# Performance work log

Measured on AMD Instinct MI355X. Metric: run time of the kernel, lower is better.

## Reference

```python
import jax, jax.numpy as jnp
import numpy as np
from jax.scipy.special import logsumexp

D = 256; H = 8; A = D // H
B_CONST = 0.9; P_MAX = 50000.0; P_MIN = 1e-4; TANH_RATE = 0.005; EPS = 1e-10
SCALE = 1.0 / np.sqrt(D)


def setup_inputs() -> dict:
    key = jax.random.key(0)
    ks = jax.random.split(key, 5)
    B, S = 2, 512
    context = jax.random.normal(ks[0], (B, S, D), dtype=jnp.float32)
    W_Q = jax.random.normal(ks[1], (D, D), dtype=jnp.float32) * (1.0 / np.sqrt(D))
    W_KV = jax.random.normal(ks[2], (2 * D, D), dtype=jnp.float32) * (1.0 / np.sqrt(D))
    W_out = jax.random.normal(ks[3], (D, D), dtype=jnp.float32) * (1.0 / np.sqrt(D))
    p_param = jax.random.normal(ks[4], (D,), dtype=jnp.float32) * 0.02
    return {"context": context, "W_Q": W_Q, "W_KV": W_KV, "W_out": W_out, "p_param": p_param}


def reference(context, W_Q, W_KV, W_out, p_param):
    B, S, _ = context.shape
    # projections (nn.Linear: x @ W.T)
    q = context @ W_Q.T                          # [B,S,D]
    kv = context @ W_KV.T                        # [B,S,2D]
    k, v = kv[..., :D], kv[..., D:]
    # scaled p: p_max*tanh(tanh_rate*p)+1, then replace exact zeros with p_min
    p = P_MAX * jnp.tanh(TANH_RATE * p_param) + 1.0
    p = p + (p == 0).astype(p.dtype) * P_MIN
    # minmax-normalize v over the key/sequence axis into [b, 1]
    v_max = jnp.max(v, axis=-2, keepdims=True)   # [B,1,D]
    v_min = jnp.min(v, axis=-2, keepdims=True)
    v = (1.0 - B_CONST) * (v - v_min) / (v_max - v_min + EPS) + B_CONST
    z = p * jnp.log(v)                           # [B,S,D]
    # split heads
    qh = q.reshape(B, S, H, A).transpose(0, 2, 1, 3)          # [B,H,S,A]
    kh = k.reshape(B, S, H, A).transpose(0, 2, 1, 3)          # [B,H,S,A]
    zh = z.reshape(B, S, H, A).transpose(0, 2, 1, 3)[:, :, None]  # [B,H,1,K,A]
    dot = jnp.einsum('bhqa,bhka->bhqk', qh, kh)
    w = jax.nn.log_softmax(dot * SCALE, axis=-1)              # [B,H,Q,K]
    # log-domain power mean: logsumexp over keys of log-weights + p*log(v)
    mean = logsumexp(w[..., None] + zh, axis=-2)              # [B,H,Q,A]
    mean = mean.transpose(0, 2, 1, 3).reshape(B, S, D)
    e = jnp.exp(mean / p)
    # invert v minmax normalization
    e = (e - B_CONST) * (v_max - v_min + EPS) / (1.0 - B_CONST) + v_min
    return e @ W_out.T
```

## Files before the change

kernel.cpp:

```cpp
#include <hip/hip_runtime.h>
#include <math.h>

#define DD 256
#define HH 8
#define AA 32
#define SS 512
#define BB 2
constexpr float BCONST      = 0.9f;
constexpr float ONE_MINUS_B = 0.1f;
constexpr float EPSF        = 1e-10f;
constexpr float SCALEF      = 0.0625f;
constexpr float FLTMAX      = 3.402823466e38f;

#define OFF_QKV    0
#define OFF_VP     786432
#define OFF_EW     1048576
#define OFF_PMIN   1310720
#define OFF_PMAX   1318912
#define OFF_VMIN   1327104
#define OFF_VRANGE 1327616
#define OFF_P      1328128

#define KB4(buf, row, col4) \
  (&(buf)[((row) << 5) | ((((col4) >> 2) ^ (((row) >> 2) & 7)) << 2)])

template<int TM, int TN, int RM, int RN, bool MM>
__global__ __launch_bounds__(256) void gemm_t(
    const float* __restrict__ A, const float* __restrict__ B0,
    const float* __restrict__ B1, int nsplit,
    float* __restrict__ C, int ldc, int K, int lda,
    float* __restrict__ pminP, float* __restrict__ pmaxP) {
  constexpr int LDT = 36;
  constexpr int CG  = TN / RN;
  constexpr int NA  = TM * 32 / 1024;
  constexpr int NB  = TN * 32 / 1024;
  __shared__ float As[TM][LDT];
  __shared__ float Bs[TN][LDT];
  const int i0 = blockIdx.x * TM;
  const int j0 = blockIdx.y * TN;
  const float* Bsrc = (j0 < nsplit) ? (B0 + (size_t)j0 * K)
                                    : (B1 + (size_t)(j0 - nsplit) * K);
  const int t  = threadIdx.x;
  const int lr = t >> 3;
  const int lc = (t & 7) << 2;
  const int tx = t % CG, ty = t / CG;

  float4 pa[NA], pb[NB];
#pragma unroll
  for (int u = 0; u < NA; ++u)
    pa[u] = *(const float4*)(A + (size_t)(i0 + lr + 32 * u) * lda + lc);
#pragma unroll
  for (int u = 0; u < NB; ++u)
    pb[u] = *(const float4*)(Bsrc + (size_t)(lr + 32 * u) * K + lc);

  float acc[RM][RN] = {};
  for (int k0 = 0; k0 < K; k0 += 32) {
    __syncthreads();
#pragma unroll
    for (int u = 0; u < NA; ++u) *(float4*)&As[lr + 32 * u][lc] = pa[u];
#pragma unroll
    for (int u = 0; u < NB; ++u) *(float4*)&Bs[lr + 32 * u][lc] = pb[u];
    __syncthreads();
    if (k0 + 32 < K) {
#pragma unroll
      for (int u = 0; u < NA; ++u)
        pa[u] = *(const float4*)(A + (size_t)(i0 + lr + 32 * u) * lda + k0 + 32 + lc);
#pragma unroll
      for (int u = 0; u < NB; ++u)
        pb[u] = *(const float4*)(Bsrc + (size_t)(lr + 32 * u) * K + k0 + 32 + lc);
    }
#pragma unroll
    for (int kk = 0; kk < 32; kk += 4) {
      float4 af[RM], bf[RN];
#pragma unroll
      for (int r = 0; r < RM; ++r) af[r] = *(const float4*)&As[ty * RM + r][kk];
#pragma unroll
      for (int c = 0; c < RN; ++c) bf[c] = *(const float4*)&Bs[tx + CG * c][kk];
#pragma unroll
      for (int r = 0; r < RM; ++r)
#pragma unroll
        for (int c = 0; c < RN; ++c)
          acc[r][c] += af[r].x * bf[c].x + af[r].y * bf[c].y +
                       af[r].z * bf[c].z + af[r].w * bf[c].w;
    }
  }
#pragma unroll
  for (int r = 0; r < RM; ++r)
#pragma unroll
    for (int c = 0; c < RN; ++c)
      C[(size_t)(i0 + ty * RM + r) * ldc + j0 + tx + CG * c] = acc[r][c];

  if (MM && j0 >= 512) {
    __syncthreads();
    float* mnb = &As[0][0];
    float* mxb = &Bs[0][0];
#pragma unroll
    for (int c = 0; c < RN; ++c) {
      float mn = acc[0][c], mx = acc[0][c];
#pragma unroll
      for (int r = 1; r < RM; ++r) {
        mn = fminf(mn, acc[r][c]);
        mx = fmaxf(mx, acc[r][c]);
      }
      mnb[(tx + CG * c) * 17 + ty] = mn;
      mxb[(tx + CG * c) * 17 + ty] = mx;
    }
    __syncthreads();
    if (t < TN) {
      float mn = mnb[t * 17], mx = mxb[t * 17];
#pragma unroll
      for (int i = 1; i < 16; ++i) {
        mn = fminf(mn, mnb[t * 17 + i]);
        mx = fmaxf(mx, mxb[t * 17 + i]);
      }
      const int bx = i0 >> 5;
      pminP[bx * 256 + (j0 - 512) + t] = mn;
      pmaxP[bx * 256 + (j0 - 512) + t] = mx;
    }
  }
}

__global__ __launch_bounds__(256) void vpk(
    const float* __restrict__ qkv, const float* __restrict__ pminP,
    const float* __restrict__ pmaxP, const float* __restrict__ p_param,
    float* __restrict__ vp, float* __restrict__ vminw,
    float* __restrict__ vrangew, float* __restrict__ pw) {
  const int blk = blockIdx.x;
  const int b = blk >> 9, s = blk & 511;
  const int d = threadIdx.x;
  float mn = pminP[(b * 16) * 256 + d];
  float mx = pmaxP[(b * 16) * 256 + d];
#pragma unroll
  for (int c = 1; c < 16; ++c) {
    mn = fminf(mn, pminP[(b * 16 + c) * 256 + d]);
    mx = fmaxf(mx, pmaxP[(b * 16 + c) * 256 + d]);
  }
  float p = 50000.0f * tanhf(0.005f * p_param[d]) + 1.0f;
  if (p == 0.0f) p = 0.0001f;
  const float range = mx - mn + EPSF;
  const float v  = qkv[((size_t)(b * 512 + s)) * 768 + 512 + d];
  const float vn = (ONE_MINUS_B * (v - mn)) / range + BCONST;
  vp[(size_t)blk * 256 + d] = expm1f(p * logf(vn));
  if (s == 0) { vminw[b * 256 + d] = mn; vrangew[b * 256 + d] = range; }
  if (blk == 0) pw[d] = p;
}

__global__ __launch_bounds__(256) void attn_k(
    const float* __restrict__ qkv, const float* __restrict__ vp,
    const float* __restrict__ pw, const float* __restrict__ vminw,
    const float* __restrict__ vrangew, float* __restrict__ ew) {
  __shared__ float qs[32][36];
  __shared__ float sc[32 * 516];
  __shared__ float kb[512 * 32];
  __shared__ float red[32];
  const int bh  = blockIdx.y;
  const int b   = bh >> 3, h = bh & 7;
  const int q0g = blockIdx.x * 32;
  const int t   = threadIdx.x;
  const int srow = t >> 3, scol4 = (t & 7) << 2;

  {
    const int q = t >> 3, c4 = (t & 7) << 2;
    float4 qv = *(const float4*)(qkv + ((size_t)(b * 512 + q0g + q)) * 768 + h * 32 + c4);
    qv.x *= SCALEF; qv.y *= SCALEF; qv.z *= SCALEF; qv.w *= SCALEF;
    *(float4*)&qs[q][c4] = qv;
  }
#pragma unroll 8
  for (int u = 0; u < 16; ++u) {
    const int r = srow + 32 * u;
    float4 v = *(const float4*)(qkv + ((size_t)(b * 512 + r)) * 768 + 256 + h * 32 + scol4);
    *(float4*)KB4(kb, r, scol4) = v;
  }
  __syncthreads();

  {
    const int qgw = t >> 6;
    const int kg  = t & 63;
    float s8[8][8] = {};
#pragma unroll 2
    for (int kk = 0; kk < 32; kk += 4) {
      float4 qf[8], kf1[4], kf2[4];
#pragma unroll
      for (int r = 0; r < 8; ++r) qf[r] = *(const float4*)&qs[qgw + 4 * r][kk];
#pragma unroll
      for (int c = 0; c < 4; ++c) {
        kf1[c] = *(const float4*)KB4(kb, kg * 4 + c, kk);
        kf2[c] = *(const float4*)KB4(kb, 256 + kg * 4 + c, kk);
      }
#pragma unroll
      for (int r = 0; r < 8; ++r)
#pragma unroll
        for (int c = 0; c < 4; ++c) {
          s8[r][c]     += qf[r].x * kf1[c].x + qf[r].y * kf1[c].y +
                          qf[r].z * kf1[c].z + qf[r].w * kf1[c].w;
          s8[r][4 + c] += qf[r].x * kf2[c].x + qf[r].y * kf2[c].y +
                          qf[r].z * kf2[c].z + qf[r].w * kf2[c].w;
        }
    }
    float rs[8];
#pragma unroll
    for (int r = 0; r < 8; ++r) {
      float s = 0.f;
#pragma unroll
      for (int c = 0; c < 8; ++c) {
        s8[r][c] = __expf(s8[r][c]);
        s += s8[r][c];
      }
      rs[r] = s;
    }
#pragma unroll
    for (int m = 1; m < 64; m <<= 1)
#pragma unroll
      for (int r = 0; r < 8; ++r) rs[r] += __shfl_xor(rs[r], m);
    if ((t & 63) == 0)
#pragma unroll
      for (int r = 0; r < 8; ++r) red[qgw + 4 * r] = rs[r];
#pragma unroll
    for (int r = 0; r < 8; ++r) {
      const int rq = qgw + 4 * r;
      *(float4*)&sc[rq * 516 + kg * 4] =
          make_float4(s8[r][0], s8[r][1], s8[r][2], s8[r][3]);
      *(float4*)&sc[rq * 516 + 256 + kg * 4] =
          make_float4(s8[r][4], s8[r][5], s8[r][6], s8[r][7]);
    }
  }
  __syncthreads();

#pragma unroll 8
  for (int u = 0; u < 16; ++u) {
    const int r = srow + 32 * u;
    float4 v = *(const float4*)(vp + ((size_t)(b * 512 + r)) * 256 + h * 32 + scol4);
    *(float4*)KB4(kb, r, scol4) = v;
  }
  __syncthreads();

  const int ag  = t & 7;
  const int qg3 = (t >> 3) & 3;
  const int ks  = t >> 5;
  float a3[8][4] = {};
#pragma unroll 2
  for (int g = 0; g < 16; ++g) {
    const int kbase = ks * 64 + g * 4;
    float4 sq[8], vf[4];
#pragma unroll
    for (int r = 0; r < 8; ++r)
      sq[r] = *(const float4*)&sc[(qg3 + 4 * r) * 516 + kbase];
#pragma unroll
    for (int c = 0; c < 4; ++c)
      vf[c] = *(const float4*)KB4(kb, kbase + c, ag * 4);
#pragma unroll
    for (int r = 0; r < 8; ++r) {
      a3[r][0] += sq[r].x * vf[0].x + sq[r].y * vf[1].x + sq[r].z * vf[2].x + sq[r].w * vf[3].x;
      a3[r][1] += sq[r].x * vf[0].y + sq[r].y * vf[1].y + sq[r].z * vf[2].y + sq[r].w * vf[3].y;
      a3[r][2] += sq[r].x * vf[0].z + sq[r].y * vf[1].z + sq[r].z * vf[2].z + sq[r].w * vf[3].z;
      a3[r][3] += sq[r].x * vf[0].w + sq[r].y * vf[1].w + sq[r].z * vf[2].w + sq[r].w * vf[3].w;
    }
  }

#pragma unroll
  for (int r = 0; r < 8; ++r)
#pragma unroll
    for (int c = 0; c < 4; ++c)
      a3[r][c] += __shfl_xor(a3[r][c], 32);
  __syncthreads();
  float* part = &kb[0];
  if ((t & 32) == 0) {
    const int w = t >> 6;
#pragma unroll
    for (int r = 0; r < 8; ++r)
#pragma unroll
      for (int c = 0; c < 4; ++c)
        part[w * 1152 + (qg3 + 4 * r) * 36 + ag * 4 + c] = a3[r][c];
  }
  __syncthreads();

  {
    const int q = t >> 3, a0 = (t & 7) << 2;
    const int d0 = h * 32 + a0;
    const float invT = 1.0f / red[q];
    float4 s0 = *(const float4*)&part[q * 36 + a0];
    float4 s1 = *(const float4*)&part[1152 + q * 36 + a0];
    float4 s2 = *(const float4*)&part[2304 + q * 36 + a0];
    float4 s3 = *(const float4*)&part[3456 + q * 36 + a0];
    const float4 pp = *(const float4*)(pw + d0);
    const float4 vr = *(const float4*)(vrangew + b * 256 + d0);
    const float4 vm = *(const float4*)(vminw + b * 256 + d0);
    float4 o;
    o.x = (expf(log1pf((s0.x + s1.x + s2.x + s3.x) * invT) / pp.x) - BCONST) * vr.x / ONE_MINUS_B + vm.x;
    o.y = (expf(log1pf((s0.y + s1.y + s2.y + s3.y) * invT) / pp.y) - BCONST) * vr.y / ONE_MINUS_B + vm.y;
    o.z = (expf(log1pf((s0.z + s1.z + s2.z + s3.z) * invT) / pp.z) - BCONST) * vr.z / ONE_MINUS_B + vm.z;
    o.w = (expf(log1pf((s0.w + s1.w + s2.w + s3.w) * invT) / pp.w) - BCONST) * vr.w / ONE_MINUS_B + vm.w;
    *(float4*)(ew + ((size_t)(b * 512 + q0g + q)) * 256 + d0) = o;
  }
}

extern "C" void kernel_launch(void* const* d_in, const int* in_sizes, int n_in,
                              void* d_out, int out_size, void* d_ws, size_t ws_size,
                              hipStream_t stream) {
  const float* ctx  = (const float*)d_in[0];
  const float* WQ   = (const float*)d_in[1];
  const float* WKV  = (const float*)d_in[2];
  const float* WOUT = (const float*)d_in[3];
  const float* PP   = (const float*)d_in[4];
  float* ws      = (float*)d_ws;
  float* qkv     = ws + OFF_QKV;
  float* vp      = ws + OFF_VP;
  float* ew      = ws + OFF_EW;
  float* pminP   = ws + OFF_PMIN;
  float* pmaxP   = ws + OFF_PMAX;
  float* vminw   = ws + OFF_VMIN;
  float* vrangew = ws + OFF_VRANGE;
  float* pw      = ws + OFF_P;
  float* out     = (float*)d_out;

  gemm_t<32, 64, 2, 4, true><<<dim3(32, 12), 256, 0, stream>>>(
      ctx, WQ, WKV, 256, qkv, 768, 256, 256, pminP, pmaxP);
  vpk<<<1024, 256, 0, stream>>>(qkv, pminP, pmaxP, PP, vp, vminw, vrangew, pw);
  attn_k<<<dim3(16, 16), 256, 0, stream>>>(qkv, vp, pw, vminw, vrangew, ew);
  gemm_t<32, 32, 2, 2, false><<<dim3(32, 8), 256, 0, stream>>>(
      ew, WOUT, WOUT, 1 << 30, out, 256, 256, 256, nullptr, nullptr);
}
```

Baseline: 107.3 us.

## Replace FP32 SIMT GEMMs with split-bf16 MFMA GEMMs

```diff
diff --git a/kernel.cpp b/kernel.cpp
--- a/kernel.cpp
+++ b/kernel.cpp
@@ -10,112 +10,133 @@
 constexpr float ONE_MINUS_B = 0.1f;
 constexpr float EPSF        = 1e-10f;
 constexpr float SCALEF      = 0.0625f;
-constexpr float FLTMAX      = 3.402823466e38f;
+
+typedef unsigned short u16;
+typedef __attribute__((ext_vector_type(4))) u16   u16x4;
+typedef __attribute__((ext_vector_type(8))) short bf16x8;
+typedef __attribute__((ext_vector_type(4))) float f32x4;
 
 #define OFF_QKV    0
 #define OFF_VP     786432
-#define OFF_EW     1048576
+#define OFF_EWH    1048576
+#define OFF_EWL    1179648
 #define OFF_PMIN   1310720
 #define OFF_PMAX   1318912
 #define OFF_VMIN   1327104
 #define OFF_VRANGE 1327616
 #define OFF_P      1328128
+#define OFF_AH     1328384
+#define OFF_AL     1459456
+#define OFF_WH     1590528
+#define OFF_WL     1688832
+#define OFF_WOH    1787136
+#define OFF_WOL    1819904
 
 #define KB4(buf, row, col4) \
   (&(buf)[((row) << 5) | ((((col4) >> 2) ^ (((row) >> 2) & 7)) << 2)])
 
-template<int TM, int TN, int RM, int RN, bool MM>
-__global__ __launch_bounds__(256) void gemm_t(
-    const float* __restrict__ A, const float* __restrict__ B0,
-    const float* __restrict__ B1, int nsplit,
-    float* __restrict__ C, int ldc, int K, int lda,
+__device__ __forceinline__ u16 f2bf(float x) {
+  unsigned u = __float_as_uint(x);
+  return (u16)((u + 0x7fffu + ((u >> 16) & 1u)) >> 16);
+}
+__device__ __forceinline__ float bf2f(u16 h) {
+  return __uint_as_float((unsigned)h << 16);
+}
+
+__device__ __forceinline__ bf16x8 ldfrag(const u16* p) {
+  u16x4 a = *(const u16x4*)p;
+  u16x4 b = *(const u16x4*)(p + 16);
+  bf16x8 r;
+  r[0] = (short)a[0]; r[1] = (short)a[1]; r[2] = (short)a[2]; r[3] = (short)a[3];
+  r[4] = (short)b[0]; r[5] = (short)b[1]; r[6] = (short)b[2]; r[7] = (short)b[3];
+  return r;
+}
+
+__global__ __launch_bounds__(256) void splitk(
+    const float* __restrict__ ctx, const float* __restrict__ WQ,
+    const float* __restrict__ WKV, const float* __restrict__ WOUT,
+    u16* __restrict__ Ah, u16* __restrict__ Al,
+    u16* __restrict__ Wh, u16* __restrict__ Wl,
+    u16* __restrict__ WOh, u16* __restrict__ WOl) {
+  const int e = (blockIdx.x * 256 + threadIdx.x) * 4;
+  const float* src; u16 *dh, *dl;
+  if (e < 262144)      { src = ctx  + e;            dh = Ah  + e;            dl = Al  + e; }
+  else if (e < 327680) { src = WQ   + (e - 262144); dh = Wh  + (e - 262144); dl = Wl  + (e - 262144); }
+  else if (e < 458752) { src = WKV  + (e - 327680); dh = Wh  + (e - 262144); dl = Wl  + (e - 262144); }
+  else                 { src = WOUT + (e - 458752); dh = WOh + (e - 458752); dl = WOl + (e - 458752); }
+  float4 v = *(const float4*)src;
+  ushort4 h, l;
+  h.x = f2bf(v.x); l.x = f2bf(v.x - bf2f(h.x));
+  h.y = f2bf(v.y); l.y = f2bf(v.y - bf2f(h.y));
+  h.z = f2bf(v.z); l.z = f2bf(v.z - bf2f(h.z));
+  h.w = f2bf(v.w); l.w = f2bf(v.w - bf2f(h.w));
+  *(ushort4*)dh = h;
+  *(ushort4*)dl = l;
+}
+
+template<int NT, bool MM>
+__global__ __launch_bounds__(256) void gemm_mfma(
+    const u16* __restrict__ Ah, const u16* __restrict__ Al,
+    const u16* __restrict__ Bh, const u16* __restrict__ Bl,
+    float* __restrict__ C, int ldc,
     float* __restrict__ pminP, float* __restrict__ pmaxP) {
-  constexpr int LDT = 36;
-  constexpr int CG  = TN / RN;
-  constexpr int NA  = TM * 32 / 1024;
-  constexpr int NB  = TN * 32 / 1024;
-  __shared__ float As[TM][LDT];
-  __shared__ float Bs[TN][LDT];
-  const int i0 = blockIdx.x * TM;
-  const int j0 = blockIdx.y * TN;
-  const float* Bsrc = (j0 < nsplit) ? (B0 + (size_t)j0 * K)
-                                    : (B1 + (size_t)(j0 - nsplit) * K);
-  const int t  = threadIdx.x;
-  const int lr = t >> 3;
-  const int lc = (t & 7) << 2;
-  const int tx = t % CG, ty = t / CG;
-
-  float4 pa[NA], pb[NB];
-#pragma unroll
-  for (int u = 0; u < NA; ++u)
-    pa[u] = *(const float4*)(A + (size_t)(i0 + lr + 32 * u) * lda + lc);
-#pragma unroll
-  for (int u = 0; u < NB; ++u)
-    pb[u] = *(const float4*)(Bsrc + (size_t)(lr + 32 * u) * K + lc);
-
-  float acc[RM][RN] = {};
-  for (int k0 = 0; k0 < K; k0 += 32) {
+  __shared__ float smn[2][64], smx[2][64];
+  const int t = threadIdx.x;
+  const int lane = t & 63, wave = t >> 6;
+  const int wm = wave >> 1, wn = wave & 1;
+  const int m = lane & 15, g = lane >> 4;
+  const int i0 = blockIdx.x * 32;
+  const int j0 = blockIdx.y * (NT * 32);
+
+  const size_t aoff = (size_t)(i0 + wm * 16 + m) * 256 + 4 * g;
+  const u16* pAh = Ah + aoff;
+  const u16* pAl = Al + aoff;
+  const u16* pBh[NT]; const u16* pBl[NT];
+#pragma unroll
+  for (int nt = 0; nt < NT; ++nt) {
+    const size_t boff = (size_t)(j0 + wn * NT * 16 + nt * 16 + m) * 256 + 4 * g;
+    pBh[nt] = Bh + boff; pBl[nt] = Bl + boff;
+  }
+
+  f32x4 acc[NT] = {};
+#pragma unroll
+  for (int k0 = 0; k0 < 256; k0 += 32) {
+    bf16x8 ah = ldfrag(pAh + k0);
+    bf16x8 al = ldfrag(pAl + k0);
+#pragma unroll
+    for (int nt = 0; nt < NT; ++nt) {
+      bf16x8 bh = ldfrag(pBh[nt] + k0);
+      bf16x8 bl = ldfrag(pBl[nt] + k0);
+      acc[nt] = __builtin_amdgcn_mfma_f32_16x16x32_bf16(ah, bh, acc[nt], 0, 0, 0);
+      acc[nt] = __builtin_amdgcn_mfma_f32_16x16x32_bf16(ah, bl, acc[nt], 0, 0, 0);
+      acc[nt] = __builtin_amdgcn_mfma_f32_16x16x32_bf16(al, bh, acc[nt], 0, 0, 0);
+    }
+  }
+
+  const int crow0 = i0 + wm * 16 + 4 * g;
+  const int ccol0 = j0 + wn * NT * 16 + m;
+#pragma unroll
+  for (int nt = 0; nt < NT; ++nt)
+#pragma unroll
+    for (int r = 0; r < 4; ++r)
+      C[(size_t)(crow0 + r) * ldc + ccol0 + nt * 16] = acc[nt][r];
+
+  if (MM && j0 >= 512) {
+#pragma unroll
+    for (int nt = 0; nt < NT; ++nt) {
+      float mn = fminf(fminf(acc[nt][0], acc[nt][1]), fminf(acc[nt][2], acc[nt][3]));
+      float mx = fmaxf(fmaxf(acc[nt][0], acc[nt][1]), fmaxf(acc[nt][2], acc[nt][3]));
+      mn = fminf(mn, __shfl_xor(mn, 16)); mx = fmaxf(mx, __shfl_xor(mx, 16));
+      mn = fminf(mn, __shfl_xor(mn, 32)); mx = fmaxf(mx, __shfl_xor(mx, 32));
+      if (g == 0) {
+        smn[wm][wn * NT * 16 + nt * 16 + m] = mn;
+        smx[wm][wn * NT * 16 + nt * 16 + m] = mx;
+      }
+    }
     __syncthreads();
-#pragma unroll
-    for (int u = 0; u < NA; ++u) *(float4*)&As[lr + 32 * u][lc] = pa[u];
-#pragma unroll
-    for (int u = 0; u < NB; ++u) *(float4*)&Bs[lr + 32 * u][lc] = pb[u];
-    __syncthreads();
-    if (k0 + 32 < K) {
-#pragma unroll
-      for (int u = 0; u < NA; ++u)
-        pa[u] = *(const float4*)(A + (size_t)(i0 + lr + 32 * u) * lda + k0 + 32 + lc);
-#pragma unroll
-      for (int u = 0; u < NB; ++u)
-        pb[u] = *(const float4*)(Bsrc + (size_t)(lr + 32 * u) * K + k0 + 32 + lc);
-    }
-#pragma unroll
-    for (int kk = 0; kk < 32; kk += 4) {
-      float4 af[RM], bf[RN];
-#pragma unroll
-      for (int r = 0; r < RM; ++r) af[r] = *(const float4*)&As[ty * RM + r][kk];
-#pragma unroll
-      for (int c = 0; c < RN; ++c) bf[c] = *(const float4*)&Bs[tx + CG * c][kk];
-#pragma unroll
-      for (int r = 0; r < RM; ++r)
-#pragma unroll
-        for (int c = 0; c < RN; ++c)
-          acc[r][c] += af[r].x * bf[c].x + af[r].y * bf[c].y +
-                       af[r].z * bf[c].z + af[r].w * bf[c].w;
-    }
-  }
-#pragma unroll
-  for (int r = 0; r < RM; ++r)
-#pragma unroll
-    for (int c = 0; c < RN; ++c)
-      C[(size_t)(i0 + ty * RM + r) * ldc + j0 + tx + CG * c] = acc[r][c];
-
-  if (MM && j0 >= 512) {
-    __syncthreads();
-    float* mnb = &As[0][0];
-    float* mxb = &Bs[0][0];
-#pragma unroll
-    for (int c = 0; c < RN; ++c) {
-      float mn = acc[0][c], mx = acc[0][c];
-#pragma unroll
-      for (int r = 1; r < RM; ++r) {
-        mn = fminf(mn, acc[r][c]);
-        mx = fmaxf(mx, acc[r][c]);
-      }
-      mnb[(tx + CG * c) * 17 + ty] = mn;
-      mxb[(tx + CG * c) * 17 + ty] = mx;
-    }
-    __syncthreads();
-    if (t < TN) {
-      float mn = mnb[t * 17], mx = mxb[t * 17];
-#pragma unroll
-      for (int i = 1; i < 16; ++i) {
-        mn = fminf(mn, mnb[t * 17 + i]);
-        mx = fmaxf(mx, mxb[t * 17 + i]);
-      }
-      const int bx = i0 >> 5;
-      pminP[bx * 256 + (j0 - 512) + t] = mn;
-      pmaxP[bx * 256 + (j0 - 512) + t] = mx;
+    if (t < NT * 32) {
+      pminP[(i0 >> 5) * 256 + (j0 - 512) + t] = fminf(smn[0][t], smn[1][t]);
+      pmaxP[(i0 >> 5) * 256 + (j0 - 512) + t] = fmaxf(smx[0][t], smx[1][t]);
     }
   }
 }
@@ -148,7 +169,8 @@
 __global__ __launch_bounds__(256) void attn_k(
     const float* __restrict__ qkv, const float* __restrict__ vp,
     const float* __restrict__ pw, const float* __restrict__ vminw,
-    const float* __restrict__ vrangew, float* __restrict__ ew) {
+    const float* __restrict__ vrangew,
+    u16* __restrict__ ewh, u16* __restrict__ ewl) {
   __shared__ float qs[32][36];
   __shared__ float sc[32 * 516];
   __shared__ float kb[512 * 32];
@@ -290,7 +312,14 @@
     o.y = (expf(log1pf((s0.y + s1.y + s2.y + s3.y) * invT) / pp.y) - BCONST) * vr.y / ONE_MINUS_B + vm.y;
     o.z = (expf(log1pf((s0.z + s1.z + s2.z + s3.z) * invT) / pp.z) - BCONST) * vr.z / ONE_MINUS_B + vm.z;
     o.w = (expf(log1pf((s0.w + s1.w + s2.w + s3.w) * invT) / pp.w) - BCONST) * vr.w / ONE_MINUS_B + vm.w;
-    *(float4*)(ew + ((size_t)(b * 512 + q0g + q)) * 256 + d0) = o;
+    ushort4 oh, ol;
+    oh.x = f2bf(o.x); ol.x = f2bf(o.x - bf2f(oh.x));
+    oh.y = f2bf(o.y); ol.y = f2bf(o.y - bf2f(oh.y));
+    oh.z = f2bf(o.z); ol.z = f2bf(o.z - bf2f(oh.z));
+    oh.w = f2bf(o.w); ol.w = f2bf(o.w - bf2f(oh.w));
+    const size_t base = ((size_t)(b * 512 + q0g + q)) * 256 + d0;
+    *(ushort4*)(ewh + base) = oh;
+    *(ushort4*)(ewl + base) = ol;
   }
 }
 
@@ -305,18 +334,26 @@
   float* ws      = (float*)d_ws;
   float* qkv     = ws + OFF_QKV;
   float* vp      = ws + OFF_VP;
-  float* ew      = ws + OFF_EW;
+  u16*   ewh     = (u16*)(ws + OFF_EWH);
+  u16*   ewl     = (u16*)(ws + OFF_EWL);
   float* pminP   = ws + OFF_PMIN;
   float* pmaxP   = ws + OFF_PMAX;
   float* vminw   = ws + OFF_VMIN;
   float* vrangew = ws + OFF_VRANGE;
   float* pw      = ws + OFF_P;
+  u16*   Ah      = (u16*)(ws + OFF_AH);
+  u16*   Al      = (u16*)(ws + OFF_AL);
+  u16*   Wh      = (u16*)(ws + OFF_WH);
+  u16*   Wl      = (u16*)(ws + OFF_WL);
+  u16*   WOh     = (u16*)(ws + OFF_WOH);
+  u16*   WOl     = (u16*)(ws + OFF_WOL);
   float* out     = (float*)d_out;
 
-  gemm_t<32, 64, 2, 4, true><<<dim3(32, 12), 256, 0, stream>>>(
-      ctx, WQ, WKV, 256, qkv, 768, 256, 256, pminP, pmaxP);
+  splitk<<<512, 256, 0, stream>>>(ctx, WQ, WKV, WOUT, Ah, Al, Wh, Wl, WOh, WOl);
+  gemm_mfma<2, true><<<dim3(32, 12), 256, 0, stream>>>(
+      Ah, Al, Wh, Wl, qkv, 768, pminP, pmaxP);
   vpk<<<1024, 256, 0, stream>>>(qkv, pminP, pmaxP, PP, vp, vminw, vrangew, pw);
-  attn_k<<<dim3(16, 16), 256, 0, stream>>>(qkv, vp, pw, vminw, vrangew, ew);
-  gemm_t<32, 32, 2, 2, false><<<dim3(32, 8), 256, 0, stream>>>(
-      ew, WOUT, WOUT, 1 << 30, out, 256, 256, 256, nullptr, nullptr);
-}
+  attn_k<<<dim3(16, 16), 256, 0, stream>>>(qkv, vp, pw, vminw, vrangew, ewh, ewl);
+  gemm_mfma<1, false><<<dim3(32, 8), 256, 0, stream>>>(
+      ewh, ewl, WOh, WOl, out, 256, nullptr, nullptr);
+}
```

New measurement: 117.4 us. 1.09x slower.

## Fuse V min/max normalization and power transform into attention kernel

Applied to the files above, without the earlier changes.

```diff
diff --git a/kernel.cpp b/kernel.cpp
--- a/kernel.cpp
+++ b/kernel.cpp
@@ -12,24 +12,17 @@
 constexpr float SCALEF      = 0.0625f;
 constexpr float FLTMAX      = 3.402823466e38f;
 
-#define OFF_QKV    0
-#define OFF_VP     786432
-#define OFF_EW     1048576
-#define OFF_PMIN   1310720
-#define OFF_PMAX   1318912
-#define OFF_VMIN   1327104
-#define OFF_VRANGE 1327616
-#define OFF_P      1328128
+#define OFF_QKV 0
+#define OFF_EW  786432
 
 #define KB4(buf, row, col4) \
   (&(buf)[((row) << 5) | ((((col4) >> 2) ^ (((row) >> 2) & 7)) << 2)])
 
-template<int TM, int TN, int RM, int RN, bool MM>
+template<int TM, int TN, int RM, int RN>
 __global__ __launch_bounds__(256) void gemm_t(
     const float* __restrict__ A, const float* __restrict__ B0,
     const float* __restrict__ B1, int nsplit,
-    float* __restrict__ C, int ldc, int K, int lda,
-    float* __restrict__ pminP, float* __restrict__ pmaxP) {
+    float* __restrict__ C, int ldc, int K, int lda) {
   constexpr int LDT = 36;
   constexpr int CG  = TN / RN;
   constexpr int NA  = TM * 32 / 1024;
@@ -89,74 +82,22 @@
 #pragma unroll
     for (int c = 0; c < RN; ++c)
       C[(size_t)(i0 + ty * RM + r) * ldc + j0 + tx + CG * c] = acc[r][c];
-
-  if (MM && j0 >= 512) {
-    __syncthreads();
-    float* mnb = &As[0][0];
-    float* mxb = &Bs[0][0];
-#pragma unroll
-    for (int c = 0; c < RN; ++c) {
-      float mn = acc[0][c], mx = acc[0][c];
-#pragma unroll
-      for (int r = 1; r < RM; ++r) {
-        mn = fminf(mn, acc[r][c]);
-        mx = fmaxf(mx, acc[r][c]);
-      }
-      mnb[(tx + CG * c) * 17 + ty] = mn;
-      mxb[(tx + CG * c) * 17 + ty] = mx;
-    }
-    __syncthreads();
-    if (t < TN) {
-      float mn = mnb[t * 17], mx = mxb[t * 17];
-#pragma unroll
-      for (int i = 1; i < 16; ++i) {
-        mn = fminf(mn, mnb[t * 17 + i]);
-        mx = fmaxf(mx, mxb[t * 17 + i]);
-      }
-      const int bx = i0 >> 5;
-      pminP[bx * 256 + (j0 - 512) + t] = mn;
-      pmaxP[bx * 256 + (j0 - 512) + t] = mx;
-    }
-  }
 }
 
-__global__ __launch_bounds__(256) void vpk(
-    const float* __restrict__ qkv, const float* __restrict__ pminP,
-    const float* __restrict__ pmaxP, const float* __restrict__ p_param,
-    float* __restrict__ vp, float* __restrict__ vminw,
-    float* __restrict__ vrangew, float* __restrict__ pw) {
-  const int blk = blockIdx.x;
-  const int b = blk >> 9, s = blk & 511;
-  const int d = threadIdx.x;
-  float mn = pminP[(b * 16) * 256 + d];
-  float mx = pmaxP[(b * 16) * 256 + d];
-#pragma unroll
-  for (int c = 1; c < 16; ++c) {
-    mn = fminf(mn, pminP[(b * 16 + c) * 256 + d]);
-    mx = fmaxf(mx, pmaxP[(b * 16 + c) * 256 + d]);
-  }
-  float p = 50000.0f * tanhf(0.005f * p_param[d]) + 1.0f;
-  if (p == 0.0f) p = 0.0001f;
-  const float range = mx - mn + EPSF;
-  const float v  = qkv[((size_t)(b * 512 + s)) * 768 + 512 + d];
-  const float vn = (ONE_MINUS_B * (v - mn)) / range + BCONST;
-  vp[(size_t)blk * 256 + d] = expm1f(p * logf(vn));
-  if (s == 0) { vminw[b * 256 + d] = mn; vrangew[b * 256 + d] = range; }
-  if (blk == 0) pw[d] = p;
-}
-
 __global__ __launch_bounds__(256) void attn_k(
-    const float* __restrict__ qkv, const float* __restrict__ vp,
-    const float* __restrict__ pw, const float* __restrict__ vminw,
-    const float* __restrict__ vrangew, float* __restrict__ ew) {
+    const float* __restrict__ qkv, const float* __restrict__ p_param,
+    float* __restrict__ ew) {
   __shared__ float qs[32][36];
   __shared__ float sc[32 * 516];
   __shared__ float kb[512 * 32];
   __shared__ float red[32];
+  __shared__ __align__(16) float wmn[128], wmx[128];
+  __shared__ __align__(16) float mnL[32], rgL[32], ivL[32], pL[32];
   const int bh  = blockIdx.y;
   const int b   = bh >> 3, h = bh & 7;
   const int q0g = blockIdx.x * 32;
   const int t   = threadIdx.x;
+  const int lane = t & 63, wave = t >> 6;
   const int srow = t >> 3, scol4 = (t & 7) << 2;
 
   {
@@ -171,7 +112,43 @@
     float4 v = *(const float4*)(qkv + ((size_t)(b * 512 + r)) * 768 + 256 + h * 32 + scol4);
     *(float4*)KB4(kb, r, scol4) = v;
   }
-  __syncthreads();
+  {
+    float4 vmn4 = make_float4(FLTMAX, FLTMAX, FLTMAX, FLTMAX);
+    float4 vmx4 = make_float4(-FLTMAX, -FLTMAX, -FLTMAX, -FLTMAX);
+#pragma unroll 4
+    for (int u = 0; u < 16; ++u) {
+      const int r = srow + 32 * u;
+      float4 v = *(const float4*)(qkv + ((size_t)(b * 512 + r)) * 768 + 512 + h * 32 + scol4);
+      vmn4.x = fminf(vmn4.x, v.x); vmx4.x = fmaxf(vmx4.x, v.x);
+      vmn4.y = fminf(vmn4.y, v.y); vmx4.y = fmaxf(vmx4.y, v.y);
+      vmn4.z = fminf(vmn4.z, v.z); vmx4.z = fmaxf(vmx4.z, v.z);
+      vmn4.w = fminf(vmn4.w, v.w); vmx4.w = fmaxf(vmx4.w, v.w);
+    }
+#pragma unroll
+    for (int m = 8; m <= 32; m <<= 1) {
+      vmn4.x = fminf(vmn4.x, __shfl_xor(vmn4.x, m)); vmx4.x = fmaxf(vmx4.x, __shfl_xor(vmx4.x, m));
+      vmn4.y = fminf(vmn4.y, __shfl_xor(vmn4.y, m)); vmx4.y = fmaxf(vmx4.y, __shfl_xor(vmx4.y, m));
+      vmn4.z = fminf(vmn4.z, __shfl_xor(vmn4.z, m)); vmx4.z = fmaxf(vmx4.z, __shfl_xor(vmx4.z, m));
+      vmn4.w = fminf(vmn4.w, __shfl_xor(vmn4.w, m)); vmx4.w = fmaxf(vmx4.w, __shfl_xor(vmx4.w, m));
+    }
+    if ((lane >> 3) == 0) {
+      *(float4*)&wmn[wave * 32 + scol4] = vmn4;
+      *(float4*)&wmx[wave * 32 + scol4] = vmx4;
+    }
+  }
+  if (t < 32) {
+    float pv = 50000.0f * tanhf(0.005f * p_param[h * 32 + t]) + 1.0f;
+    if (pv == 0.0f) pv = 0.0001f;
+    pL[t] = pv;
+  }
+  __syncthreads();
+
+  if (t < 32) {
+    float mn = fminf(fminf(wmn[t], wmn[32 + t]), fminf(wmn[64 + t], wmn[96 + t]));
+    float mx = fmaxf(fmaxf(wmx[t], wmx[32 + t]), fmaxf(wmx[64 + t], wmx[96 + t]));
+    const float rg = mx - mn + EPSF;
+    mnL[t] = mn; rgL[t] = rg; ivL[t] = ONE_MINUS_B / rg;
+  }
 
   {
     const int qgw = t >> 6;
@@ -226,11 +203,20 @@
   }
   __syncthreads();
 
-#pragma unroll 8
-  for (int u = 0; u < 16; ++u) {
-    const int r = srow + 32 * u;
-    float4 v = *(const float4*)(vp + ((size_t)(b * 512 + r)) * 256 + h * 32 + scol4);
-    *(float4*)KB4(kb, r, scol4) = v;
+  {
+    const float4 mnv = *(const float4*)&mnL[scol4];
+    const float4 ivv = *(const float4*)&ivL[scol4];
+    const float4 pv4 = *(const float4*)&pL[scol4];
+#pragma unroll 4
+    for (int u = 0; u < 16; ++u) {
+      const int r = srow + 32 * u;
+      float4 v = *(const float4*)(qkv + ((size_t)(b * 512 + r)) * 768 + 512 + h * 32 + scol4);
+      v.x = expm1f(pv4.x * logf(ivv.x * (v.x - mnv.x) + BCONST));
+      v.y = expm1f(pv4.y * logf(ivv.y * (v.y - mnv.y) + BCONST));
+      v.z = expm1f(pv4.z * logf(ivv.z * (v.z - mnv.z) + BCONST));
+      v.w = expm1f(pv4.w * logf(ivv.w * (v.w - mnv.w) + BCONST));
+      *(float4*)KB4(kb, r, scol4) = v;
+    }
   }
   __syncthreads();
 
@@ -282,9 +268,9 @@
     float4 s1 = *(const float4*)&part[1152 + q * 36 + a0];
     float4 s2 = *(const float4*)&part[2304 + q * 36 + a0];
     float4 s3 = *(const float4*)&part[3456 + q * 36 + a0];
-    const float4 pp = *(const float4*)(pw + d0);
-    const float4 vr = *(const float4*)(vrangew + b * 256 + d0);
-    const float4 vm = *(const float4*)(vminw + b * 256 + d0);
+    const float4 pp = *(const float4*)&pL[a0];
+    const float4 vr = *(const float4*)&rgL[a0];
+    const float4 vm = *(const float4*)&mnL[a0];
     float4 o;
     o.x = (expf(log1pf((s0.x + s1.x + s2.x + s3.x) * invT) / pp.x) - BCONST) * vr.x / ONE_MINUS_B + vm.x;
     o.y = (expf(log1pf((s0.y + s1.y + s2.y + s3.y) * invT) / pp.y) - BCONST) * vr.y / ONE_MINUS_B + vm.y;
@@ -302,21 +288,14 @@
   const float* WKV  = (const float*)d_in[2];
   const float* WOUT = (const float*)d_in[3];
   const float* PP   = (const float*)d_in[4];
-  float* ws      = (float*)d_ws;
-  float* qkv     = ws + OFF_QKV;
-  float* vp      = ws + OFF_VP;
-  float* ew      = ws + OFF_EW;
-  float* pminP   = ws + OFF_PMIN;
-  float* pmaxP   = ws + OFF_PMAX;
-  float* vminw   = ws + OFF_VMIN;
-  float* vrangew = ws + OFF_VRANGE;
-  float* pw      = ws + OFF_P;
-  float* out     = (float*)d_out;
-
-  gemm_t<32, 64, 2, 4, true><<<dim3(32, 12), 256, 0, stream>>>(
-      ctx, WQ, WKV, 256, qkv, 768, 256, 256, pminP, pmaxP);
-  vpk<<<1024, 256, 0, stream>>>(qkv, pminP, pmaxP, PP, vp, vminw, vrangew, pw);
-  attn_k<<<dim3(16, 16), 256, 0, stream>>>(qkv, vp, pw, vminw, vrangew, ew);
-  gemm_t<32, 32, 2, 2, false><<<dim3(32, 8), 256, 0, stream>>>(
-      ew, WOUT, WOUT, 1 << 30, out, 256, 256, 256, nullptr, nullptr);
+  float* ws  = (float*)d_ws;
+  float* qkv = ws + OFF_QKV;
+  float* ew  = ws + OFF_EW;
+  float* out = (float*)d_out;
+
+  gemm_t<32, 64, 2, 4><<<dim3(32, 12), 256, 0, stream>>>(
+      ctx, WQ, WKV, 256, qkv, 768, 256, 256);
+  attn_k<<<dim3(16, 16), 256, 0, stream>>>(qkv, PP, ew);
+  gemm_t<32, 32, 2, 2><<<dim3(32, 8), 256, 0, stream>>>(
+      ew, WOUT, WOUT, 1 << 30, out, 256, 256, 256);
 }
```

Result: slower. 109.8 us (+2.3%).
